# Kernel optimization log

Hardware: AMD Instinct MI355X
Metric: run time of the kernel (lower is better)

Reference implementation:

```python
import jax, jax.numpy as jnp
import numpy as np

IN_FEATURES = 4096
OUT_FEATURES = 4096
RANK = 16
SCALING = 1.0  # lora_alpha / r = 16 / 16


def setup_inputs() -> dict:
    key = jax.random.key(0)
    k1, k2, k3, k4 = jax.random.split(key, 4)
    x = jax.random.normal(k1, (4, 2048, IN_FEATURES), dtype=jnp.float32)
    # packed weight: (out_features, in_features // 4), repeated x4 at forward time
    weight_packed = jax.random.normal(k2, (OUT_FEATURES, IN_FEATURES // 4), dtype=jnp.float32) * 0.02
    lora_A = jax.random.normal(k3, (RANK, IN_FEATURES), dtype=jnp.float32) * 0.02
    lora_B = jax.random.normal(k4, (OUT_FEATURES, RANK), dtype=jnp.float32) * 0.02
    return {"x": x, "weight_packed": weight_packed, "lora_A": lora_A, "lora_B": lora_B, "scaling": 1}


def reference(x, weight_packed, lora_A, lora_B, scaling):
    W = jnp.tile(weight_packed, (1, 4))  # [out, in]
    base = jnp.einsum('bsi,oi->bso', x, W)
    # LoRA low-rank path: (x @ A^T) @ B^T * scaling
    lora = jnp.einsum('bsr,or->bso', jnp.einsum('bsi,ri->bsr', x, lora_A), lora_B)
    return base + lora * jnp.float32(scaling)
```

## Files before the change

kernel.cpp:

```cpp
#include <hip/hip_runtime.h>
#include <hip/hip_bf16.h>
#include <stdint.h>

#define M_DIM 8192
#define N_DIM 4096
#define K_DIM 4096
#define RANK  16

#define BM 256
#define BN 256
#define BK 64
#define NKT (K_DIM / BK)

typedef __attribute__((ext_vector_type(8))) __bf16 bf16x8;
typedef __attribute__((ext_vector_type(4))) float  f32x4;
typedef __attribute__((ext_vector_type(8))) unsigned short u16x8;

__device__ __forceinline__ unsigned short f2bf(float f) {
    union { float f; uint32_t u; } c; c.f = f;
    uint32_t b = c.u;
    b += 0x7FFFu + ((b >> 16) & 1u);
    return (unsigned short)(b >> 16);
}

#define WEFF_BLOCKS 1024
#define CONV_BLOCKS 2048
__global__ __launch_bounds__(256) void prep_kernel(
    const float* __restrict__ x,
    const float* __restrict__ wp,
    const float* __restrict__ lA,
    const float* __restrict__ lB,
    const int*   __restrict__ scaling,
    unsigned short* __restrict__ xb,
    unsigned short* __restrict__ weff) {
    __shared__ float lAs[16][512];
    const int t = threadIdx.x;
    if (blockIdx.x < WEFF_BLOCKS) {
        const int bo = blockIdx.x >> 3;
        const int bi = blockIdx.x & 7;
#pragma unroll
        for (int v = 0; v < 8; ++v) {
            int idx = v * 256 + t;
            int r = idx >> 7;
            int c4 = idx & 127;
            reinterpret_cast<float4*>(&lAs[r][0])[c4] =
                reinterpret_cast<const float4*>(lA + (size_t)r * 4096 + bi * 512)[c4];
        }
        __syncthreads();
        const int row = t >> 3;
        const int o = bo * 32 + row;
        const float s = (float)scaling[0];
        float b[RANK];
#pragma unroll
        for (int r = 0; r < RANK; ++r) b[r] = lB[o * RANK + r] * s;
        const float* wrow = wp + (size_t)o * 1024;
        const int cbase = (t & 7) * 4;
#pragma unroll
        for (int j = 0; j < 16; ++j) {
            int c = cbase + j * 32;
            int gi = bi * 512 + c;
            float4 w = *reinterpret_cast<const float4*>(wrow + (gi & 1023));
            float a0 = w.x, a1 = w.y, a2 = w.z, a3 = w.w;
#pragma unroll
            for (int r = 0; r < RANK; ++r) {
                float4 la = *reinterpret_cast<const float4*>(&lAs[r][c]);
                a0 = fmaf(b[r], la.x, a0);
                a1 = fmaf(b[r], la.y, a1);
                a2 = fmaf(b[r], la.z, a2);
                a3 = fmaf(b[r], la.w, a3);
            }
            ushort4 ov;
            ov.x = f2bf(a0); ov.y = f2bf(a1); ov.z = f2bf(a2); ov.w = f2bf(a3);
            *reinterpret_cast<ushort4*>(weff + (size_t)o * 4096 + gi) = ov;
        }
    } else {
        const int n8 = (M_DIM * K_DIM) / 8;
        int idx = (blockIdx.x - WEFF_BLOCKS) * 256 + t;
        const int stride = CONV_BLOCKS * 256;
        for (int i = idx; i < n8; i += stride) {
            float4 v0 = reinterpret_cast<const float4*>(x)[2 * i];
            float4 v1 = reinterpret_cast<const float4*>(x)[2 * i + 1];
            u16x8 o;
            o[0] = f2bf(v0.x); o[1] = f2bf(v0.y); o[2] = f2bf(v0.z); o[3] = f2bf(v0.w);
            o[4] = f2bf(v1.x); o[5] = f2bf(v1.y); o[6] = f2bf(v1.z); o[7] = f2bf(v1.w);
            reinterpret_cast<u16x8*>(xb)[i] = o;
        }
    }
}


template<int MH, int NH>
__device__ __forceinline__ void mfma_quad(const bf16x8 (&a)[4][2], const bf16x8 (&b)[2][2],
                                          f32x4 (&acc)[8][4]) {
#pragma unroll
    for (int kc = 0; kc < 2; ++kc)
#pragma unroll
        for (int mf = 0; mf < 4; ++mf)
#pragma unroll
            for (int nf = 0; nf < 2; ++nf)
                acc[MH * 4 + mf][NH * 2 + nf] = __builtin_amdgcn_mfma_f32_16x16x32_bf16(
                    a[mf][kc], b[nf][kc], acc[MH * 4 + mf][NH * 2 + nf], 0, 0, 0);
}

__global__ __launch_bounds__(512, 1) void gemm_kernel(
    const unsigned short* __restrict__ A,
    const unsigned short* __restrict__ B,
    float* __restrict__ C)
{
    __shared__ __align__(16) char lds[131072];

    const int tid  = threadIdx.x;
    const int lane = tid & 63;
    const int wave = tid >> 6;
    const int wr = wave >> 2;
    const int wc = wave & 3;

    const int bid = blockIdx.x;
    const int swz = (bid & 7) * 64 + (bid >> 3);
    const int bm = swz >> 4;
    const int bn = swz & 15;
    const int m0 = bm * BM;
    const int n0 = bn * BN;

    const int srccol = 8 * ((tid & 7) ^ ((tid >> 3) & 7));
    const int wub    = (tid & ~63) * 16;
    const unsigned short* Ag = A + (size_t)(m0 + (tid >> 3)) * K_DIM + srccol;
    const unsigned short* Bg = B + (size_t)(n0 + (tid >> 8) * 64 + ((tid >> 3) & 31)) * K_DIM + srccol;

#define STAGE_A(buf, mh, kt) do { \
    __builtin_amdgcn_global_load_lds( \
        (const __attribute__((address_space(1))) void*)(Ag + (size_t)((mh) * 64) * K_DIM + (size_t)(kt) * 64), \
        (__attribute__((address_space(3))) void*)(lds + (buf) * 65536 + (mh) * 16384 + wub), 16, 0, 0); \
    __builtin_amdgcn_global_load_lds( \
        (const __attribute__((address_space(1))) void*)(Ag + (size_t)(128 + (mh) * 64) * K_DIM + (size_t)(kt) * 64), \
        (__attribute__((address_space(3))) void*)(lds + (buf) * 65536 + (mh) * 16384 + 8192 + wub), 16, 0, 0); \
} while (0)

#define STAGE_B(buf, nh, kt) do { \
    __builtin_amdgcn_global_load_lds( \
        (const __attribute__((address_space(1))) void*)(Bg + (size_t)((nh) * 32) * K_DIM + (size_t)(kt) * 64), \
        (__attribute__((address_space(3))) void*)(lds + (buf) * 65536 + 32768 + (nh) * 16384 + wub), 16, 0, 0); \
    __builtin_amdgcn_global_load_lds( \
        (const __attribute__((address_space(1))) void*)(Bg + (size_t)(128 + (nh) * 32) * K_DIM + (size_t)(kt) * 64), \
        (__attribute__((address_space(3))) void*)(lds + (buf) * 65536 + 32768 + (nh) * 16384 + 8192 + wub), 16, 0, 0); \
} while (0)

    const int wrA   = wr * 8192;
    const int wcB   = wc * 4096;
    const int rdrow = (lane & 15) * 128;
    const int rdxor = (lane & 7) << 4;
    const int rdg   = (lane >> 4) * 16;

#define RD_A(dst, buf, mh) do { \
    _Pragma("unroll") for (int mf = 0; mf < 4; ++mf) \
    _Pragma("unroll") for (int kc = 0; kc < 2; ++kc) \
        dst[mf][kc] = *(const bf16x8*)(lds + (buf) * 65536 + (mh) * 16384 + wrA + rdrow + mf * 2048 + ((kc * 64 + rdg) ^ rdxor)); \
} while (0)

#define RD_B(dst, buf, nh) do { \
    _Pragma("unroll") for (int nf = 0; nf < 2; ++nf) \
    _Pragma("unroll") for (int kc = 0; kc < 2; ++kc) \
        dst[nf][kc] = *(const bf16x8*)(lds + (buf) * 65536 + 32768 + (nh) * 16384 + wcB + rdrow + nf * 2048 + ((kc * 64 + rdg) ^ rdxor)); \
} while (0)

#define PH_TAIL(QUAD) \
    __builtin_amdgcn_s_barrier(); \
    asm volatile("s_waitcnt lgkmcnt(0)" ::: "memory"); \
    __builtin_amdgcn_s_setprio(1); \
    QUAD; \
    __builtin_amdgcn_s_setprio(0);

    f32x4 acc[8][4];
#pragma unroll
    for (int i = 0; i < 8; ++i)
#pragma unroll
        for (int j = 0; j < 4; ++j) acc[i][j] = (f32x4){0.f, 0.f, 0.f, 0.f};

    bf16x8 afr[4][2];
    bf16x8 b0[2][2], b1[2][2];

    STAGE_A(0, 0, 0); STAGE_B(0, 1, 0); STAGE_A(0, 1, 0); STAGE_B(0, 0, 0);
    STAGE_A(1, 0, 1); STAGE_B(1, 1, 1);
    asm volatile("s_waitcnt vmcnt(4)" ::: "memory");
    __builtin_amdgcn_s_barrier();

    for (int it = 0; it < NKT / 2; ++it) {
        const int k1 = 2 * it + 1;
        const int k2 = (2 * it + 2) & (NKT - 1);
        const int k3 = (2 * it + 3) & (NKT - 1);

        RD_A(afr, 0, 0); RD_B(b0, 0, 0);
        STAGE_A(1, 1, k1);
        asm volatile("s_waitcnt lgkmcnt(8)" ::: "memory");
        PH_TAIL((mfma_quad<0, 0>(afr, b0, acc)));
        RD_B(b1, 0, 1);
        STAGE_B(1, 0, k1);
        PH_TAIL((mfma_quad<0, 1>(afr, b1, acc)));
        RD_A(afr, 0, 1);
        STAGE_A(0, 0, k2);
        PH_TAIL((mfma_quad<1, 1>(afr, b1, acc)));
        STAGE_B(0, 1, k2);
        PH_TAIL((mfma_quad<1, 0>(afr, b0, acc)));
        asm volatile("s_waitcnt vmcnt(4)" ::: "memory");
        __builtin_amdgcn_s_barrier();
        RD_A(afr, 1, 0); RD_B(b0, 1, 0);
        STAGE_A(0, 1, k2);
        asm volatile("s_waitcnt lgkmcnt(8)" ::: "memory");
        PH_TAIL((mfma_quad<0, 0>(afr, b0, acc)));
        RD_B(b1, 1, 1);
        STAGE_B(0, 0, k2);
        PH_TAIL((mfma_quad<0, 1>(afr, b1, acc)));
        RD_A(afr, 1, 1);
        STAGE_A(1, 0, k3);
        PH_TAIL((mfma_quad<1, 1>(afr, b1, acc)));
        STAGE_B(1, 1, k3);
        PH_TAIL((mfma_quad<1, 0>(afr, b0, acc)));
        asm volatile("s_waitcnt vmcnt(4)" ::: "memory");
        __builtin_amdgcn_s_barrier();
    }

    {
        float* lsc = (float*)lds + wave * (16 * 84);
        const int wcol  = lane & 15;
        const int wrow4 = (lane >> 4) * 4;
        const int rrow  = lane >> 3;
        const int rcol  = (lane & 7) * 4;
        const int crow0 = m0 + wr * 128;
        const int ccol0 = n0 + wc * 64;
#pragma unroll
        for (int mi = 0; mi < 8; ++mi) {
#pragma unroll
            for (int ni = 0; ni < 4; ++ni)
#pragma unroll
                for (int r = 0; r < 4; ++r)
                    lsc[(wrow4 + r) * 84 + ni * 16 + wcol] = acc[mi][ni][r];
            asm volatile("s_waitcnt lgkmcnt(0)" ::: "memory");
#pragma unroll
            for (int rh = 0; rh < 2; ++rh)
#pragma unroll
                for (int j = 0; j < 2; ++j) {
                    f32x4 v = *(const f32x4*)&lsc[(rh * 8 + rrow) * 84 + rcol + j * 32];
                    *(f32x4*)&C[(size_t)(crow0 + mi * 16 + rh * 8 + rrow) * N_DIM +
                                ccol0 + rcol + j * 32] = v;
                }
            asm volatile("s_waitcnt lgkmcnt(0)" ::: "memory");
        }
    }

#undef STAGE_A
#undef STAGE_B
#undef RD_A
#undef RD_B
#undef PH_TAIL
}

extern "C" void kernel_launch(void* const* d_in, const int* in_sizes, int n_in,
                              void* d_out, int out_size, void* d_ws, size_t ws_size,
                              hipStream_t stream) {
    const float* x  = (const float*)d_in[0];
    const float* wp = (const float*)d_in[1];
    const float* lA = (const float*)d_in[2];
    const float* lB = (const float*)d_in[3];
    const int*   sc = (const int*)d_in[4];
    float* out = (float*)d_out;

    unsigned short* xb   = (unsigned short*)d_ws;
    unsigned short* weff = (unsigned short*)d_ws + (size_t)M_DIM * K_DIM;

    prep_kernel<<<WEFF_BLOCKS + CONV_BLOCKS, 256, 0, stream>>>(x, wp, lA, lB, sc, xb, weff);

    int grid = (M_DIM / BM) * (N_DIM / BN);
    gemm_kernel<<<grid, 512, 0, stream>>>(xb, weff, out);
}
```

Measured before the change: 271.2 us.

## Switch GEMM to 32x32x16 MFMA with fragment-ordered LDS layout

```diff
diff --git a/kernel.cpp b/kernel.cpp
--- a/kernel.cpp
+++ b/kernel.cpp
@@ -12,9 +12,9 @@
 #define BK 64
 #define NKT (K_DIM / BK)
 
-typedef __attribute__((ext_vector_type(8))) __bf16 bf16x8;
-typedef __attribute__((ext_vector_type(4))) float  f32x4;
-typedef __attribute__((ext_vector_type(8))) unsigned short u16x8;
+typedef __attribute__((ext_vector_type(8)))  __bf16 bf16x8;
+typedef __attribute__((ext_vector_type(16))) float  f32x16;
+typedef __attribute__((ext_vector_type(8)))  unsigned short u16x8;
 
 __device__ __forceinline__ unsigned short f2bf(float f) {
     union { float f; uint32_t u; } c; c.f = f;
@@ -90,16 +90,14 @@
 
 
 template<int MH, int NH>
-__device__ __forceinline__ void mfma_quad(const bf16x8 (&a)[4][2], const bf16x8 (&b)[2][2],
-                                          f32x4 (&acc)[8][4]) {
-#pragma unroll
-    for (int kc = 0; kc < 2; ++kc)
-#pragma unroll
-        for (int mf = 0; mf < 4; ++mf)
-#pragma unroll
-            for (int nf = 0; nf < 2; ++nf)
-                acc[MH * 4 + mf][NH * 2 + nf] = __builtin_amdgcn_mfma_f32_16x16x32_bf16(
-                    a[mf][kc], b[nf][kc], acc[MH * 4 + mf][NH * 2 + nf], 0, 0, 0);
+__device__ __forceinline__ void mfma_quad(const bf16x8 (&a)[2][4], const bf16x8 (&b)[4],
+                                          f32x16 (&acc)[4][2]) {
+#pragma unroll
+    for (int kc = 0; kc < 4; ++kc)
+#pragma unroll
+        for (int mti = 0; mti < 2; ++mti)
+            acc[MH * 2 + mti][NH] = __builtin_amdgcn_mfma_f32_32x32x16_bf16(
+                a[mti][kc], b[kc], acc[MH * 2 + mti][NH], 0, 0, 0);
 }
 
 __global__ __launch_bounds__(512, 1) void gemm_kernel(
@@ -111,9 +109,9 @@
 
     const int tid  = threadIdx.x;
     const int lane = tid & 63;
-    const int wave = tid >> 6;
-    const int wr = wave >> 2;
-    const int wc = wave & 3;
+    const int w    = tid >> 6;
+    const int wr = w >> 2;
+    const int wc = w & 3;
 
     const int bid = blockIdx.x;
     const int swz = (bid & 7) * 64 + (bid >> 3);
@@ -122,45 +120,42 @@
     const int m0 = bm * BM;
     const int n0 = bn * BN;
 
-    const int srccol = 8 * ((tid & 7) ^ ((tid >> 3) & 7));
-    const int wub    = (tid & ~63) * 16;
-    const unsigned short* Ag = A + (size_t)(m0 + (tid >> 3)) * K_DIM + srccol;
-    const unsigned short* Bg = B + (size_t)(n0 + (tid >> 8) * 64 + ((tid >> 3) & 31)) * K_DIM + srccol;
+    const unsigned short* Asrc = A + (size_t)(m0 + (lane & 31)) * K_DIM + (lane >> 5) * 8;
+    const unsigned short* Bsrc = B + (size_t)(n0 + (lane & 31)) * K_DIM + (lane >> 5) * 8;
 
 #define STAGE_A(buf, mh, kt) do { \
-    __builtin_amdgcn_global_load_lds( \
-        (const __attribute__((address_space(1))) void*)(Ag + (size_t)((mh) * 64) * K_DIM + (size_t)(kt) * 64), \
-        (__attribute__((address_space(3))) void*)(lds + (buf) * 65536 + (mh) * 16384 + wub), 16, 0, 0); \
-    __builtin_amdgcn_global_load_lds( \
-        (const __attribute__((address_space(1))) void*)(Ag + (size_t)(128 + (mh) * 64) * K_DIM + (size_t)(kt) * 64), \
-        (__attribute__((address_space(3))) void*)(lds + (buf) * 65536 + (mh) * 16384 + 8192 + wub), 16, 0, 0); \
+    _Pragma("unroll") for (int j = 0; j < 2; ++j) { \
+        const int f_ = j * 8 + w, q_ = f_ >> 2, kc_ = f_ & 3; \
+        const int mt_ = (mh) * 2 + (q_ & 1) + (q_ >> 1) * 4; \
+        __builtin_amdgcn_global_load_lds( \
+            (const __attribute__((address_space(1))) void*)(Asrc + (size_t)(mt_ * 32) * K_DIM + (kt) * 64 + kc_ * 16), \
+            (__attribute__((address_space(3))) void*)(lds + (buf) * 65536 + mt_ * 4096 + kc_ * 1024), 16, 0, 0); \
+    } \
 } while (0)
 
 #define STAGE_B(buf, nh, kt) do { \
-    __builtin_amdgcn_global_load_lds( \
-        (const __attribute__((address_space(1))) void*)(Bg + (size_t)((nh) * 32) * K_DIM + (size_t)(kt) * 64), \
-        (__attribute__((address_space(3))) void*)(lds + (buf) * 65536 + 32768 + (nh) * 16384 + wub), 16, 0, 0); \
-    __builtin_amdgcn_global_load_lds( \
-        (const __attribute__((address_space(1))) void*)(Bg + (size_t)(128 + (nh) * 32) * K_DIM + (size_t)(kt) * 64), \
-        (__attribute__((address_space(3))) void*)(lds + (buf) * 65536 + 32768 + (nh) * 16384 + 8192 + wub), 16, 0, 0); \
-} while (0)
-
-    const int wrA   = wr * 8192;
-    const int wcB   = wc * 4096;
-    const int rdrow = (lane & 15) * 128;
-    const int rdxor = (lane & 7) << 4;
-    const int rdg   = (lane >> 4) * 16;
+    _Pragma("unroll") for (int j = 0; j < 2; ++j) { \
+        const int f_ = j * 8 + w, q_ = f_ >> 2, kc_ = f_ & 3; \
+        const int nt_ = 2 * q_ + (nh); \
+        __builtin_amdgcn_global_load_lds( \
+            (const __attribute__((address_space(1))) void*)(Bsrc + (size_t)(nt_ * 32) * K_DIM + (kt) * 64 + kc_ * 16), \
+            (__attribute__((address_space(3))) void*)(lds + (buf) * 65536 + 32768 + nt_ * 4096 + kc_ * 1024), 16, 0, 0); \
+    } \
+} while (0)
+
+    const int lb = lane * 16;
+    const int wr4 = wr * 4;
+    const int wc2 = wc * 2;
 
 #define RD_A(dst, buf, mh) do { \
-    _Pragma("unroll") for (int mf = 0; mf < 4; ++mf) \
-    _Pragma("unroll") for (int kc = 0; kc < 2; ++kc) \
-        dst[mf][kc] = *(const bf16x8*)(lds + (buf) * 65536 + (mh) * 16384 + wrA + rdrow + mf * 2048 + ((kc * 64 + rdg) ^ rdxor)); \
+    _Pragma("unroll") for (int mti = 0; mti < 2; ++mti) \
+    _Pragma("unroll") for (int kc = 0; kc < 4; ++kc) \
+        dst[mti][kc] = *(const bf16x8*)(lds + (buf) * 65536 + (wr4 + (mh) * 2 + mti) * 4096 + kc * 1024 + lb); \
 } while (0)
 
 #define RD_B(dst, buf, nh) do { \
-    _Pragma("unroll") for (int nf = 0; nf < 2; ++nf) \
-    _Pragma("unroll") for (int kc = 0; kc < 2; ++kc) \
-        dst[nf][kc] = *(const bf16x8*)(lds + (buf) * 65536 + 32768 + (nh) * 16384 + wcB + rdrow + nf * 2048 + ((kc * 64 + rdg) ^ rdxor)); \
+    _Pragma("unroll") for (int kc = 0; kc < 4; ++kc) \
+        dst[kc] = *(const bf16x8*)(lds + (buf) * 65536 + 32768 + (wc2 + (nh)) * 4096 + kc * 1024 + lb); \
 } while (0)
 
 #define PH_TAIL(QUAD) \
@@ -170,14 +165,16 @@
     QUAD; \
     __builtin_amdgcn_s_setprio(0);
 
-    f32x4 acc[8][4];
-#pragma unroll
-    for (int i = 0; i < 8; ++i)
-#pragma unroll
-        for (int j = 0; j < 4; ++j) acc[i][j] = (f32x4){0.f, 0.f, 0.f, 0.f};
-
-    bf16x8 afr[4][2];
-    bf16x8 b0[2][2], b1[2][2];
+    f32x16 acc[4][2];
+#pragma unroll
+    for (int i = 0; i < 4; ++i)
+#pragma unroll
+        for (int j = 0; j < 2; ++j)
+#pragma unroll
+            for (int r = 0; r < 16; ++r) acc[i][j][r] = 0.f;
+
+    bf16x8 afr[2][4];
+    bf16x8 b0[4], b1[4];
 
     STAGE_A(0, 0, 0); STAGE_B(0, 1, 0); STAGE_A(0, 1, 0); STAGE_B(0, 0, 0);
     STAGE_A(1, 0, 1); STAGE_B(1, 1, 1);
@@ -219,33 +216,16 @@
         __builtin_amdgcn_s_barrier();
     }
 
-    {
-        float* lsc = (float*)lds + wave * (16 * 84);
-        const int wcol  = lane & 15;
-        const int wrow4 = (lane >> 4) * 4;
-        const int rrow  = lane >> 3;
-        const int rcol  = (lane & 7) * 4;
-        const int crow0 = m0 + wr * 128;
-        const int ccol0 = n0 + wc * 64;
-#pragma unroll
-        for (int mi = 0; mi < 8; ++mi) {
-#pragma unroll
-            for (int ni = 0; ni < 4; ++ni)
-#pragma unroll
-                for (int r = 0; r < 4; ++r)
-                    lsc[(wrow4 + r) * 84 + ni * 16 + wcol] = acc[mi][ni][r];
-            asm volatile("s_waitcnt lgkmcnt(0)" ::: "memory");
-#pragma unroll
-            for (int rh = 0; rh < 2; ++rh)
-#pragma unroll
-                for (int j = 0; j < 2; ++j) {
-                    f32x4 v = *(const f32x4*)&lsc[(rh * 8 + rrow) * 84 + rcol + j * 32];
-                    *(f32x4*)&C[(size_t)(crow0 + mi * 16 + rh * 8 + rrow) * N_DIM +
-                                ccol0 + rcol + j * 32] = v;
-                }
-            asm volatile("s_waitcnt lgkmcnt(0)" ::: "memory");
-        }
-    }
+    const int crow = m0 + wr * 128 + 4 * (lane >> 5);
+    const int ccol = n0 + wc * 64 + (lane & 31);
+#pragma unroll
+    for (int mt = 0; mt < 4; ++mt)
+#pragma unroll
+        for (int nt = 0; nt < 2; ++nt)
+#pragma unroll
+            for (int r = 0; r < 16; ++r)
+                C[(size_t)(crow + mt * 32 + (r & 3) + 8 * (r >> 2)) * N_DIM + ccol + nt * 32] =
+                    acc[mt][nt][r];
 
 #undef STAGE_A
 #undef STAGE_B
```

Result: slower. 391.9 us (+44.5%).
